# Optimization experiments

Measured on AMD Instinct MI355X. Metric: run time of the kernel, lower is better.

The kernel has to match this reference:

```python
import jax, jax.numpy as jnp
import numpy as np

N = 50000      # nodes
E = 800000     # edges (avg degree 16)
DF = 128       # node feature dim
EF = 16        # edge feature dim
EH = 64        # edge_filters
NH = 128       # node_filters
C = 40         # classes


def setup_inputs() -> dict:
    key = jax.random.key(0)
    ks = jax.random.split(key, 11)
    s = lambda fan_in: 1.0 / np.sqrt(fan_in)
    return {
        "x": jax.random.normal(ks[0], (N, DF), jnp.float32),
        "edge_feat": jax.random.normal(ks[1], (E, EF), jnp.float32),
        "W1": jax.random.normal(ks[2], (EF, EH), jnp.float32) * s(EF),
        "b1": jnp.zeros((EH,), jnp.float32),
        "W2": jax.random.normal(ks[3], (EH, 1), jnp.float32) * s(EH),
        "b2": jnp.zeros((1,), jnp.float32),
        "Wc1": jax.random.normal(ks[4], (DF, NH), jnp.float32) * s(DF),
        "bc1": jnp.zeros((NH,), jnp.float32),
        "Wc2": jax.random.normal(ks[5], (NH, C), jnp.float32) * s(NH),
        "bc2": jnp.zeros((C,), jnp.float32),
        "edge_index": jax.random.randint(ks[6], (2, E), 0, N, jnp.int32),
    }


def reference(x, edge_feat, W1, b1, W2, b2, Wc1, bc1, Wc2, bc2, edge_index):
    # Edge MLP: per-edge scalar weight in (0, 1)
    eh = jnp.maximum(edge_feat @ W1 + b1, 0.0)          # [E, EH] relu
    ew = jax.nn.sigmoid(eh @ W2 + b2)[:, 0]             # [E]

    # SparseTensor(edges.T, ew, (n, n)): indices are (row=dst, col=src)
    dst = edge_index[0]
    src = edge_index[1]

    # GCNConv 1: relu(A @ (x @ Wc1) + bc1)
    h = x @ Wc1                                         # [N, NH]
    msg = h[src] * ew[:, None]                          # [E, NH] gather
    agg = jax.ops.segment_sum(msg, dst, num_segments=N) # [N, NH] scatter
    h1 = jnp.maximum(agg + bc1, 0.0)
    # dropout(training=False) is identity

    # GCNConv 2: A @ (h1 @ Wc2) + bc2 (linear activation)
    h2 = h1 @ Wc2                                       # [N, C]
    msg2 = h2[src] * ew[:, None]                        # [E, C]
    agg2 = jax.ops.segment_sum(msg2, dst, num_segments=N) + bc2

    return -jax.nn.log_softmax(agg2, axis=1)            # [N, C]
```

## Files before the change

### kernel.cpp

```cpp
#include <hip/hip_runtime.h>
#include <math.h>

#define N_NODES 50000
#define N_EDGES 800000
#define DF 128
#define EF 16
#define EH 64
#define NH 128
#define NC 40
#define SCAN_B 196

__global__ __launch_bounds__(256) void edge_mlp_kernel(
    const float* __restrict__ ef, const float* __restrict__ W1,
    const float* __restrict__ b1, const float* __restrict__ W2,
    const float* __restrict__ b2, const int* __restrict__ dst,
    float* __restrict__ ew, int* __restrict__ deg)
{
    __shared__ float4 W1s4[EF * 16];
    __shared__ float4 b1s4[16];
    __shared__ float4 W2s4[16];
    int t = threadIdx.x;
    for (int i = t; i < EF * 16; i += 256) W1s4[i] = ((const float4*)W1)[i];
    if (t < 16) { b1s4[t] = ((const float4*)b1)[t]; W2s4[t] = ((const float4*)W2)[t]; }
    __syncthreads();

    int e = blockIdx.x * 256 + t;
    if (e >= N_EDGES) return;

    float f[EF];
    const float4* ef4 = (const float4*)(ef + (long)e * EF);
    #pragma unroll
    for (int i = 0; i < 4; ++i) {
        float4 v = ef4[i];
        f[4*i+0] = v.x; f[4*i+1] = v.y; f[4*i+2] = v.z; f[4*i+3] = v.w;
    }
    float s = 0.f;
    #pragma unroll 4
    for (int jc = 0; jc < 16; ++jc) {
        float4 a = b1s4[jc];
        #pragma unroll
        for (int k = 0; k < EF; ++k) {
            float4 w = W1s4[k * 16 + jc];
            a.x += f[k] * w.x; a.y += f[k] * w.y;
            a.z += f[k] * w.z; a.w += f[k] * w.w;
        }
        float4 w2 = W2s4[jc];
        s += fmaxf(a.x, 0.f) * w2.x + fmaxf(a.y, 0.f) * w2.y
           + fmaxf(a.z, 0.f) * w2.z + fmaxf(a.w, 0.f) * w2.w;
    }
    s += b2[0];
    ew[e] = 1.f / (1.f + expf(-s));
    atomicAdd(&deg[dst[e]], 1);
}

__global__ __launch_bounds__(256) void gemm1_kernel(
    const float* __restrict__ x, const float* __restrict__ Wc1,
    float* __restrict__ h)
{
    __shared__ float xs[64][DF];
    int t = threadIdx.x;
    long r0 = (long)blockIdx.x * 64;
    for (int i = t; i < 64 * DF; i += 256) {
        int r = i >> 7, k = i & 127;
        long rr = r0 + r;
        xs[r][k] = (rr < N_NODES) ? x[rr * DF + k] : 0.f;
    }
    __syncthreads();

    int tr = t >> 5;
    int tc = t & 31;
    float acc[8][4];
    #pragma unroll
    for (int i = 0; i < 8; ++i)
        #pragma unroll
        for (int j = 0; j < 4; ++j) acc[i][j] = 0.f;

    #pragma unroll 2
    for (int k = 0; k < DF; ++k) {
        float4 w = *(const float4*)(Wc1 + k * NH + tc * 4);
        float xv[8];
        #pragma unroll
        for (int i = 0; i < 8; ++i) xv[i] = xs[tr * 8 + i][k];
        #pragma unroll
        for (int i = 0; i < 8; ++i) {
            acc[i][0] += xv[i] * w.x;
            acc[i][1] += xv[i] * w.y;
            acc[i][2] += xv[i] * w.z;
            acc[i][3] += xv[i] * w.w;
        }
    }
    #pragma unroll
    for (int i = 0; i < 8; ++i) {
        long r = r0 + tr * 8 + i;
        if (r < N_NODES)
            *(float4*)(h + r * NH + tc * 4) =
                make_float4(acc[i][0], acc[i][1], acc[i][2], acc[i][3]);
    }
}

__global__ __launch_bounds__(256) void scan_part_kernel(
    const int* __restrict__ deg, int* __restrict__ bsum)
{
    __shared__ int red[256];
    int t = threadIdx.x;
    int n = blockIdx.x * 256 + t;
    red[t] = (n < N_NODES) ? deg[n] : 0;
    __syncthreads();
    for (int o = 128; o > 0; o >>= 1) {
        if (t < o) red[t] += red[t + o];
        __syncthreads();
    }
    if (t == 0) bsum[blockIdx.x] = red[0];
}

__global__ __launch_bounds__(256) void scan_top_kernel(
    const int* __restrict__ bsum, int* __restrict__ boff)
{
    __shared__ int s[256];
    int t = threadIdx.x;
    s[t] = (t < SCAN_B) ? bsum[t] : 0;
    __syncthreads();
    for (int o = 1; o < 256; o <<= 1) {
        int v = (t >= o) ? s[t - o] : 0;
        __syncthreads();
        s[t] += v;
        __syncthreads();
    }
    if (t < SCAN_B) boff[t] = (t == 0) ? 0 : s[t - 1];
}

__global__ __launch_bounds__(256) void scan_write_kernel(
    const int* __restrict__ deg, const int* __restrict__ boff,
    int* __restrict__ rowptr)
{
    __shared__ int s[256];
    int t = threadIdx.x;
    int n = blockIdx.x * 256 + t;
    int v = (n < N_NODES) ? deg[n] : 0;
    s[t] = v;
    __syncthreads();
    for (int o = 1; o < 256; o <<= 1) {
        int u = (t >= o) ? s[t - o] : 0;
        __syncthreads();
        s[t] += u;
        __syncthreads();
    }
    if (n < N_NODES) rowptr[n] = boff[blockIdx.x] + s[t] - v;
}

__global__ __launch_bounds__(256) void fill_csr_kernel(
    const int* __restrict__ dst, const int* __restrict__ src,
    const float* __restrict__ ew, int* __restrict__ rowptr,
    int* __restrict__ csr_src, float* __restrict__ csr_ew)
{
    int e = blockIdx.x * 256 + threadIdx.x;
    if (e >= N_EDGES) return;
    int p = atomicAdd(&rowptr[dst[e]], 1);
    csr_src[p] = src[e];
    csr_ew[p]  = ew[e];
}

__global__ __launch_bounds__(256) void gather1_gemm2_kernel(
    const float* __restrict__ h, const int* __restrict__ rp_end,
    const int* __restrict__ csr_src, const float* __restrict__ csr_ew,
    const float* __restrict__ bc1, const float* __restrict__ Wc2,
    float* __restrict__ h2)
{
    __shared__ float h1s[4][NH + 1];
    int t = threadIdx.x;
    int wv = t >> 6, lane = t & 63;
    int node = blockIdx.x * 4 + wv;

    int end   = rp_end[node];
    int start = (node == 0) ? 0 : rp_end[node - 1];
    float2 acc = make_float2(0.f, 0.f);
    for (int base = start; base < end; base += 64) {
        int n = min(64, end - base);
        int s = 0; float w = 0.f;
        if (base + lane < end) {
            s = csr_src[base + lane];
            w = csr_ew[base + lane];
        }
        #pragma unroll 4
        for (int j = 0; j < n; ++j) {
            int   sj = __shfl(s, j, 64);
            float wj = __shfl(w, j, 64);
            float2 v = *(const float2*)(h + (long)sj * NH + lane * 2);
            acc.x += wj * v.x;
            acc.y += wj * v.y;
        }
    }
    h1s[wv][lane * 2 + 0] = fmaxf(acc.x + bc1[lane * 2 + 0], 0.f);
    h1s[wv][lane * 2 + 1] = fmaxf(acc.y + bc1[lane * 2 + 1], 0.f);
    __syncthreads();

    if (t < 4 * NC) {
        int nn = t / NC, c = t - nn * NC;
        float a0 = 0.f, a1 = 0.f;
        #pragma unroll 4
        for (int k = 0; k < NH; k += 2) {
            a0 += h1s[nn][k]     * Wc2[k * NC + c];
            a1 += h1s[nn][k + 1] * Wc2[(k + 1) * NC + c];
        }
        h2[(long)(blockIdx.x * 4 + nn) * NC + c] = a0 + a1;
    }
}

__global__ __launch_bounds__(256) void gather2_lsm_kernel(
    const float* __restrict__ h2, const int* __restrict__ rp_end,
    const int* __restrict__ csr_src, const float* __restrict__ csr_ew,
    const float* __restrict__ bc2, float* __restrict__ out)
{
    int wid  = (blockIdx.x * 256 + threadIdx.x) >> 6;
    int lane = threadIdx.x & 63;
    int end   = rp_end[wid];
    int start = (wid == 0) ? 0 : rp_end[wid - 1];
    float acc = 0.f;
    for (int base = start; base < end; base += 64) {
        int n = min(64, end - base);
        int s = 0; float w = 0.f;
        if (base + lane < end) {
            s = csr_src[base + lane];
            w = csr_ew[base + lane];
        }
        #pragma unroll 4
        for (int j = 0; j < n; ++j) {
            int   sj = __shfl(s, j, 64);
            float wj = __shfl(w, j, 64);
            float v = (lane < NC) ? h2[(long)sj * NC + lane] : 0.f;
            acc += wj * v;
        }
    }
    float v = (lane < NC) ? acc + bc2[lane] : -INFINITY;
    float m = v;
    #pragma unroll
    for (int o = 32; o > 0; o >>= 1) m = fmaxf(m, __shfl_xor(m, o, 64));
    float ex = (lane < NC) ? expf(v - m) : 0.f;
    float ssum = ex;
    #pragma unroll
    for (int o = 32; o > 0; o >>= 1) ssum += __shfl_xor(ssum, o, 64);
    float lse = m + logf(ssum);
    if (lane < NC) out[(long)wid * NC + lane] = lse - v;
}

extern "C" void kernel_launch(void* const* d_in, const int* in_sizes, int n_in,
                              void* d_out, int out_size, void* d_ws, size_t ws_size,
                              hipStream_t stream)
{
    const float* x         = (const float*)d_in[0];
    const float* edge_feat = (const float*)d_in[1];
    const float* W1        = (const float*)d_in[2];
    const float* b1        = (const float*)d_in[3];
    const float* W2        = (const float*)d_in[4];
    const float* b2        = (const float*)d_in[5];
    const float* Wc1       = (const float*)d_in[6];
    const float* bc1       = (const float*)d_in[7];
    const float* Wc2       = (const float*)d_in[8];
    const float* bc2       = (const float*)d_in[9];
    const int*   eidx      = (const int*)d_in[10];
    const int*   dst = eidx;
    const int*   src = eidx + N_EDGES;
    float* out = (float*)d_out;

    float* ew      = (float*)d_ws;
    float* h       = ew + N_EDGES;
    float* h2      = h + (long)N_NODES * NH;
    int*   csr_src = (int*)(h2 + (long)N_NODES * NC);
    float* csr_ew  = (float*)(csr_src + N_EDGES);
    int*   deg     = (int*)(csr_ew + N_EDGES);
    int*   rowptr  = deg + N_NODES;
    int*   bsum    = rowptr + N_NODES;
    int*   boff    = bsum + 256;

    hipMemsetAsync(deg, 0, sizeof(int) * (size_t)N_NODES, stream);

    edge_mlp_kernel<<<(N_EDGES + 255) / 256, 256, 0, stream>>>(
        edge_feat, W1, b1, W2, b2, dst, ew, deg);
    gemm1_kernel<<<(N_NODES + 63) / 64, 256, 0, stream>>>(x, Wc1, h);
    scan_part_kernel<<<SCAN_B, 256, 0, stream>>>(deg, bsum);
    scan_top_kernel<<<1, 256, 0, stream>>>(bsum, boff);
    scan_write_kernel<<<SCAN_B, 256, 0, stream>>>(deg, boff, rowptr);
    fill_csr_kernel<<<(N_EDGES + 255) / 256, 256, 0, stream>>>(
        dst, src, ew, rowptr, csr_src, csr_ew);
    gather1_gemm2_kernel<<<N_NODES / 4, 256, 0, stream>>>(
        h, rowptr, csr_src, csr_ew, bc1, Wc2, h2);
    gather2_lsm_kernel<<<(N_NODES * 64) / 256, 256, 0, stream>>>(
        h2, rowptr, csr_src, csr_ew, bc2, out);
}
```

Measured before the change: 417.1 us.

## Store node features in bf16, pack CSR pairs, and gather four edges per wavefront

The intermediate node features h and h2 are now stored as bf16 (h2 padded to 64 columns), which halves the bytes moved by the random-access gathers. The CSR source index and edge weight are packed into one int2 so each edge needs a single load. Each wavefront now processes four edges at once with 16-byte row loads and then reduces across lane groups. The second small GEMM uses shuffles in place of shared memory and a sync. The cost is bf16 rounding error in the intermediates and extra cross-lane reduction work.

```diff
diff --git a/kernel.cpp b/kernel.cpp
--- a/kernel.cpp
+++ b/kernel.cpp
@@ -8,7 +8,20 @@
 #define EH 64
 #define NH 128
 #define NC 40
+#define NCP 64
 #define SCAN_B 196
+
+typedef __attribute__((ext_vector_type(8))) short short8v;
+typedef __attribute__((ext_vector_type(4))) short short4v;
+
+__device__ __forceinline__ float bf2f(unsigned short u) {
+    union { unsigned int i; float f; } c; c.i = ((unsigned int)u) << 16; return c.f;
+}
+__device__ __forceinline__ unsigned short f2bf(float f) {
+    union { float f; unsigned int i; } c; c.f = f;
+    unsigned int r = c.i + 0x7FFFu + ((c.i >> 16) & 1u);
+    return (unsigned short)(r >> 16);
+}
 
 __global__ __launch_bounds__(256) void edge_mlp_kernel(
     const float* __restrict__ ef, const float* __restrict__ W1,
@@ -55,7 +68,7 @@
 
 __global__ __launch_bounds__(256) void gemm1_kernel(
     const float* __restrict__ x, const float* __restrict__ Wc1,
-    float* __restrict__ h)
+    unsigned short* __restrict__ hb)
 {
     __shared__ float xs[64][DF];
     int t = threadIdx.x;
@@ -92,9 +105,12 @@
     #pragma unroll
     for (int i = 0; i < 8; ++i) {
         long r = r0 + tr * 8 + i;
-        if (r < N_NODES)
-            *(float4*)(h + r * NH + tc * 4) =
-                make_float4(acc[i][0], acc[i][1], acc[i][2], acc[i][3]);
+        if (r < N_NODES) {
+            ushort4 sv;
+            sv.x = f2bf(acc[i][0]); sv.y = f2bf(acc[i][1]);
+            sv.z = f2bf(acc[i][2]); sv.w = f2bf(acc[i][3]);
+            *(ushort4*)(hb + r * NH + tc * 4) = sv;
+        }
     }
 }
 
@@ -151,96 +167,132 @@
 __global__ __launch_bounds__(256) void fill_csr_kernel(
     const int* __restrict__ dst, const int* __restrict__ src,
     const float* __restrict__ ew, int* __restrict__ rowptr,
-    int* __restrict__ csr_src, float* __restrict__ csr_ew)
+    int2* __restrict__ csr)
 {
     int e = blockIdx.x * 256 + threadIdx.x;
     if (e >= N_EDGES) return;
     int p = atomicAdd(&rowptr[dst[e]], 1);
-    csr_src[p] = src[e];
-    csr_ew[p]  = ew[e];
+    csr[p] = make_int2(src[e], __float_as_int(ew[e]));
 }
 
 __global__ __launch_bounds__(256) void gather1_gemm2_kernel(
-    const float* __restrict__ h, const int* __restrict__ rp_end,
-    const int* __restrict__ csr_src, const float* __restrict__ csr_ew,
-    const float* __restrict__ bc1, const float* __restrict__ Wc2,
-    float* __restrict__ h2)
-{
-    __shared__ float h1s[4][NH + 1];
-    int t = threadIdx.x;
-    int wv = t >> 6, lane = t & 63;
-    int node = blockIdx.x * 4 + wv;
+    const unsigned short* __restrict__ hb, const int* __restrict__ rp_end,
+    const int2* __restrict__ csr, const float* __restrict__ bc1,
+    const float* __restrict__ Wc2, unsigned short* __restrict__ h2b)
+{
+    int t = threadIdx.x;
+    int node = blockIdx.x * 4 + (t >> 6);
+    int lane = t & 63;
+    int l16 = lane & 15, g = lane >> 4;
 
     int end   = rp_end[node];
     int start = (node == 0) ? 0 : rp_end[node - 1];
-    float2 acc = make_float2(0.f, 0.f);
+
+    float acc[8];
+    #pragma unroll
+    for (int i = 0; i < 8; ++i) acc[i] = 0.f;
+
     for (int base = start; base < end; base += 64) {
-        int n = min(64, end - base);
+        int n = end - base; if (n > 64) n = 64;
         int s = 0; float w = 0.f;
-        if (base + lane < end) {
-            s = csr_src[base + lane];
-            w = csr_ew[base + lane];
+        if (lane < n) {
+            int2 p = csr[base + lane];
+            s = p.x; w = __int_as_float(p.y);
         }
         #pragma unroll 4
-        for (int j = 0; j < n; ++j) {
-            int   sj = __shfl(s, j, 64);
-            float wj = __shfl(w, j, 64);
-            float2 v = *(const float2*)(h + (long)sj * NH + lane * 2);
-            acc.x += wj * v.x;
-            acc.y += wj * v.y;
-        }
-    }
-    h1s[wv][lane * 2 + 0] = fmaxf(acc.x + bc1[lane * 2 + 0], 0.f);
-    h1s[wv][lane * 2 + 1] = fmaxf(acc.y + bc1[lane * 2 + 1], 0.f);
-    __syncthreads();
-
-    if (t < 4 * NC) {
-        int nn = t / NC, c = t - nn * NC;
-        float a0 = 0.f, a1 = 0.f;
+        for (int j = 0; j * 4 < n; ++j) {
+            int idx = j * 4 + g;
+            int   sj = __shfl(s, idx, 64);
+            float wj = __shfl(w, idx, 64);
+            short8v hv = *(const short8v*)(hb + (long)sj * NH + l16 * 8);
+            #pragma unroll
+            for (int i = 0; i < 8; ++i)
+                acc[i] += wj * bf2f((unsigned short)hv[i]);
+        }
+    }
+    #pragma unroll
+    for (int i = 0; i < 8; ++i) {
+        acc[i] += __shfl_xor(acc[i], 16, 64);
+        acc[i] += __shfl_xor(acc[i], 32, 64);
+    }
+    float4 b0 = *(const float4*)(bc1 + l16 * 8);
+    float4 b1 = *(const float4*)(bc1 + l16 * 8 + 4);
+    float h1v[8];
+    h1v[0] = fmaxf(acc[0] + b0.x, 0.f); h1v[1] = fmaxf(acc[1] + b0.y, 0.f);
+    h1v[2] = fmaxf(acc[2] + b0.z, 0.f); h1v[3] = fmaxf(acc[3] + b0.w, 0.f);
+    h1v[4] = fmaxf(acc[4] + b1.x, 0.f); h1v[5] = fmaxf(acc[5] + b1.y, 0.f);
+    h1v[6] = fmaxf(acc[6] + b1.z, 0.f); h1v[7] = fmaxf(acc[7] + b1.w, 0.f);
+
+    int c = (lane < NC) ? lane : (NC - 1);
+    float o = 0.f;
+    #pragma unroll 8
+    for (int k = 0; k < NH; ++k) {
+        float hk = __shfl(h1v[k & 7], k >> 3, 64);
+        o += hk * Wc2[k * NC + c];
+    }
+    h2b[(long)node * NCP + lane] = f2bf((lane < NC) ? o : 0.f);
+}
+
+__global__ __launch_bounds__(256) void gather2_lsm_kernel(
+    const unsigned short* __restrict__ h2b, const int* __restrict__ rp_end,
+    const int2* __restrict__ csr, const float* __restrict__ bc2,
+    float* __restrict__ out)
+{
+    int t = threadIdx.x;
+    int node = blockIdx.x * 4 + (t >> 6);
+    int lane = t & 63;
+    int l16 = lane & 15, g = lane >> 4;
+
+    int end   = rp_end[node];
+    int start = (node == 0) ? 0 : rp_end[node - 1];
+
+    float acc[4];
+    #pragma unroll
+    for (int i = 0; i < 4; ++i) acc[i] = 0.f;
+
+    for (int base = start; base < end; base += 64) {
+        int n = end - base; if (n > 64) n = 64;
+        int s = 0; float w = 0.f;
+        if (lane < n) {
+            int2 p = csr[base + lane];
+            s = p.x; w = __int_as_float(p.y);
+        }
         #pragma unroll 4
-        for (int k = 0; k < NH; k += 2) {
-            a0 += h1s[nn][k]     * Wc2[k * NC + c];
-            a1 += h1s[nn][k + 1] * Wc2[(k + 1) * NC + c];
-        }
-        h2[(long)(blockIdx.x * 4 + nn) * NC + c] = a0 + a1;
-    }
-}
-
-__global__ __launch_bounds__(256) void gather2_lsm_kernel(
-    const float* __restrict__ h2, const int* __restrict__ rp_end,
-    const int* __restrict__ csr_src, const float* __restrict__ csr_ew,
-    const float* __restrict__ bc2, float* __restrict__ out)
-{
-    int wid  = (blockIdx.x * 256 + threadIdx.x) >> 6;
-    int lane = threadIdx.x & 63;
-    int end   = rp_end[wid];
-    int start = (wid == 0) ? 0 : rp_end[wid - 1];
-    float acc = 0.f;
-    for (int base = start; base < end; base += 64) {
-        int n = min(64, end - base);
-        int s = 0; float w = 0.f;
-        if (base + lane < end) {
-            s = csr_src[base + lane];
-            w = csr_ew[base + lane];
-        }
-        #pragma unroll 4
-        for (int j = 0; j < n; ++j) {
-            int   sj = __shfl(s, j, 64);
-            float wj = __shfl(w, j, 64);
-            float v = (lane < NC) ? h2[(long)sj * NC + lane] : 0.f;
-            acc += wj * v;
-        }
-    }
-    float v = (lane < NC) ? acc + bc2[lane] : -INFINITY;
-    float m = v;
-    #pragma unroll
-    for (int o = 32; o > 0; o >>= 1) m = fmaxf(m, __shfl_xor(m, o, 64));
-    float ex = (lane < NC) ? expf(v - m) : 0.f;
-    float ssum = ex;
-    #pragma unroll
-    for (int o = 32; o > 0; o >>= 1) ssum += __shfl_xor(ssum, o, 64);
-    float lse = m + logf(ssum);
-    if (lane < NC) out[(long)wid * NC + lane] = lse - v;
+        for (int j = 0; j * 4 < n; ++j) {
+            int idx = j * 4 + g;
+            int   sj = __shfl(s, idx, 64);
+            float wj = __shfl(w, idx, 64);
+            short4v hv = *(const short4v*)(h2b + (long)sj * NCP + l16 * 4);
+            #pragma unroll
+            for (int i = 0; i < 4; ++i)
+                acc[i] += wj * bf2f((unsigned short)hv[i]);
+        }
+    }
+    #pragma unroll
+    for (int i = 0; i < 4; ++i) {
+        acc[i] += __shfl_xor(acc[i], 16, 64);
+        acc[i] += __shfl_xor(acc[i], 32, 64);
+    }
+
+    bool valid = (l16 < 10);
+    float4 bcv = valid ? *(const float4*)(bc2 + l16 * 4) : make_float4(0.f, 0.f, 0.f, 0.f);
+    float v[4];
+    v[0] = acc[0] + bcv.x; v[1] = acc[1] + bcv.y;
+    v[2] = acc[2] + bcv.z; v[3] = acc[3] + bcv.w;
+
+    float mx = valid ? fmaxf(fmaxf(v[0], v[1]), fmaxf(v[2], v[3])) : -INFINITY;
+    #pragma unroll
+    for (int o = 1; o <= 8; o <<= 1) mx = fmaxf(mx, __shfl_xor(mx, o, 64));
+    float se = 0.f;
+    if (valid) se = expf(v[0]-mx) + expf(v[1]-mx) + expf(v[2]-mx) + expf(v[3]-mx);
+    #pragma unroll
+    for (int o = 1; o <= 8; o <<= 1) se += __shfl_xor(se, o, 64);
+    float lse = mx + logf(se);
+
+    if (valid && g == 0) {
+        float4 r = make_float4(lse - v[0], lse - v[1], lse - v[2], lse - v[3]);
+        *(float4*)(out + (long)node * NC + l16 * 4) = r;
+    }
 }
 
 extern "C" void kernel_launch(void* const* d_in, const int* in_sizes, int n_in,
@@ -262,28 +314,27 @@
     const int*   src = eidx + N_EDGES;
     float* out = (float*)d_out;
 
-    float* ew      = (float*)d_ws;
-    float* h       = ew + N_EDGES;
-    float* h2      = h + (long)N_NODES * NH;
-    int*   csr_src = (int*)(h2 + (long)N_NODES * NC);
-    float* csr_ew  = (float*)(csr_src + N_EDGES);
-    int*   deg     = (int*)(csr_ew + N_EDGES);
-    int*   rowptr  = deg + N_NODES;
-    int*   bsum    = rowptr + N_NODES;
-    int*   boff    = bsum + 256;
+    float*          ew     = (float*)d_ws;
+    unsigned short* hb     = (unsigned short*)(ew + N_EDGES);
+    unsigned short* h2b    = hb + (long)N_NODES * NH;
+    int2*           csr    = (int2*)(h2b + (long)N_NODES * NCP);
+    int*            deg    = (int*)(csr + N_EDGES);
+    int*            rowptr = deg + N_NODES;
+    int*            bsum   = rowptr + N_NODES;
+    int*            boff   = bsum + 256;
 
     hipMemsetAsync(deg, 0, sizeof(int) * (size_t)N_NODES, stream);
 
     edge_mlp_kernel<<<(N_EDGES + 255) / 256, 256, 0, stream>>>(
         edge_feat, W1, b1, W2, b2, dst, ew, deg);
-    gemm1_kernel<<<(N_NODES + 63) / 64, 256, 0, stream>>>(x, Wc1, h);
+    gemm1_kernel<<<(N_NODES + 63) / 64, 256, 0, stream>>>(x, Wc1, hb);
     scan_part_kernel<<<SCAN_B, 256, 0, stream>>>(deg, bsum);
     scan_top_kernel<<<1, 256, 0, stream>>>(bsum, boff);
     scan_write_kernel<<<SCAN_B, 256, 0, stream>>>(deg, boff, rowptr);
     fill_csr_kernel<<<(N_EDGES + 255) / 256, 256, 0, stream>>>(
-        dst, src, ew, rowptr, csr_src, csr_ew);
+        dst, src, ew, rowptr, csr);
     gather1_gemm2_kernel<<<N_NODES / 4, 256, 0, stream>>>(
-        h, rowptr, csr_src, csr_ew, bc1, Wc2, h2);
-    gather2_lsm_kernel<<<(N_NODES * 64) / 256, 256, 0, stream>>>(
-        h2, rowptr, csr_src, csr_ew, bc2, out);
-}
+        hb, rowptr, csr, bc1, Wc2, h2b);
+    gather2_lsm_kernel<<<N_NODES / 4, 256, 0, stream>>>(
+        h2b, rowptr, csr, bc2, out);
+}
```

New measurement: 367.8 us. 11.8% less time.
